# Kernel tuning notes

Hardware: AMD Instinct MI355X
Metric: run time of the kernel (lower is better)

## Reference

```python
import jax, jax.numpy as jnp
import numpy as np

B, N, C = 16, 1025, 1024
H, D = 16, 64          # num_heads, head_dim
NPT = 1                # num_prefix_tokens
EPS = 1e-6
SCALE = D ** -0.5


def layer_norm(x, g, b, eps=EPS):
    mu = jnp.mean(x, axis=-1, keepdims=True)
    var = jnp.mean(jnp.square(x - mu), axis=-1, keepdims=True)
    return (x - mu) * jax.lax.rsqrt(var + eps) * g + b


def rot(x):
    # interleaved rotate-half: out[..., ::2] = -x[..., 1::2]; out[..., 1::2] = x[..., ::2]
    x2 = x.reshape(*x.shape[:-1], -1, 2)
    return jnp.stack([-x2[..., 1], x2[..., 0]], axis=-1).reshape(x.shape)


def apply_rot_embed_cat(x, emb):
    # emb: (N_spatial, 2*D) = [sin | cos]
    sin_emb, cos_emb = jnp.split(emb, 2, axis=-1)
    return x * cos_emb + rot(x) * sin_emb


def setup_inputs() -> dict:
    key = jax.random.key(0)
    ks = jax.random.split(key, 12)
    s = 0.02
    return {
        "x": jax.random.normal(ks[0], (B, N, C), jnp.float32),
        "rope": jax.random.normal(ks[1], (N - NPT, 2 * D), jnp.float32),
        "qkv_w": jax.random.normal(ks[2], (3 * C, C), jnp.float32) * s,
        "q_bias": jax.random.normal(ks[3], (C,), jnp.float32) * s,
        "k_bias": jnp.zeros((C,), jnp.float32),  # registered buffer, always zero
        "v_bias": jax.random.normal(ks[4], (C,), jnp.float32) * s,
        "qn_g": jnp.ones((D,), jnp.float32),
        "qn_b": jnp.zeros((D,), jnp.float32),
        "kn_g": jnp.ones((D,), jnp.float32),
        "kn_b": jnp.zeros((D,), jnp.float32),
        "norm_g": jnp.ones((C,), jnp.float32),
        "norm_b": jnp.zeros((C,), jnp.float32),
        "proj_w": jax.random.normal(ks[5], (C, C), jnp.float32) * s,
        "proj_b": jnp.zeros((C,), jnp.float32),
    }


def reference(x, rope, qkv_w, q_bias, k_bias, v_bias, qn_g, qn_b, kn_g, kn_b,
              norm_g, norm_b, proj_w, proj_b):
    b, n, c = x.shape
    qkv_bias = jnp.concatenate([q_bias, k_bias, v_bias])
    qkv = jnp.einsum('bnc,oc->bno', x, qkv_w) + qkv_bias          # (B,N,3C)
    qkv = qkv.reshape(b, n, 3, H, D).transpose(2, 0, 3, 1, 4)     # (3,B,H,N,D)
    q, k, v = qkv[0], qkv[1], qkv[2]
    # per-head QK layernorm over head_dim
    q = layer_norm(q, qn_g, qn_b)
    k = layer_norm(k, kn_g, kn_b)
    # RoPE on spatial tokens only (prefix tokens excluded)
    q = jnp.concatenate([q[:, :, :NPT], apply_rot_embed_cat(q[:, :, NPT:], rope)], axis=2)
    k = jnp.concatenate([k[:, :, :NPT], apply_rot_embed_cat(k[:, :, NPT:], rope)], axis=2)
    # scaled dot product attention
    attn = jnp.einsum('bhqd,bhkd->bhqk', q * SCALE, k)
    attn = jax.nn.softmax(attn, axis=-1)
    out = jnp.einsum('bhqk,bhkd->bhqd', attn, v)                  # (B,H,N,D)
    out = out.transpose(0, 2, 1, 3).reshape(b, n, c)              # (B,N,C)
    out = layer_norm(out, norm_g, norm_b)                         # scale_norm
    out = jnp.einsum('bnc,oc->bno', out, proj_w) + proj_b
    return out
```

## Files before the change

kernel.cpp:

```cpp
#include <hip/hip_runtime.h>
#include <hip/hip_bf16.h>

#define B_ 16
#define N_ 1025
#define C_ 1024
#define H_ 16
#define D_ 64
#define M_ (B_ * N_)
#define EPS_ 1e-6f
#define SCALE_ 0.125f
#define VTS_ 1088

typedef __attribute__((ext_vector_type(8))) short bf16x8;
typedef __attribute__((ext_vector_type(4))) float f32x4;
typedef unsigned short u16;
typedef unsigned int u32;

__device__ inline float bf2f(u16 h) {
    union { u32 u; float f; } c; c.u = ((u32)h) << 16; return c.f;
}
__device__ inline u16 f2bf(float f) {
    union { u32 u; float f; } c; c.f = f;
    u32 r = c.u + 0x7FFF + ((c.u >> 16) & 1);
    return (u16)(r >> 16);
}
__device__ inline u32 cvtpk(float lo, float hi) {
    u32 r;
    asm("v_cvt_pk_bf16_f32 %0, %1, %2" : "=v"(r) : "v"(lo), "v"(hi));
    return r;
}

__device__ inline void gload16(const void* g, void* l) {
    __builtin_amdgcn_global_load_lds(
        (const __attribute__((address_space(1))) void*)g,
        (__attribute__((address_space(3))) void*)l, 16, 0, 0);
}

__global__ void k_sniff(const u32* __restrict__ norm_g_bits, int* __restrict__ flag)
{
    if (threadIdx.x == 0 && blockIdx.x == 0)
        flag[0] = (norm_g_bits[0] == 0x3F800000u) ? 1 : 0;
}

__global__ __launch_bounds__(256) void k_convert(
    const void* __restrict__ src, u16* __restrict__ dst, long n,
    const int* __restrict__ flag)
{
    const int f = flag[0];
    long i0 = ((long)blockIdx.x * 256 + threadIdx.x) * 4;
    long stride = (long)gridDim.x * 1024;
    if (f) {
        const float* s = (const float*)src;
        for (long i = i0; i < n; i += stride) {
#pragma unroll
            for (int j = 0; j < 4; ++j) dst[i + j] = f2bf(s[i + j]);
        }
    } else {
        const u16* s = (const u16*)src;
        for (long i = i0; i < n; i += stride) {
#pragma unroll
            for (int j = 0; j < 4; ++j) dst[i + j] = s[i + j];
        }
    }
}

__global__ __launch_bounds__(256) void k_convert_small(
    const void* s0, const void* s1, const void* s2, const void* s3,
    const void* s4, const void* s5, const void* s6, const void* s7,
    const void* s8, const void* s9, u16* __restrict__ dst,
    const int* __restrict__ flag)
{
    int i = blockIdx.x * 256 + threadIdx.x;
    if (i >= 6400) return;
    const void* src; int off;
    if      (i < 1024) { src = s0; off = i; }
    else if (i < 2048) { src = s1; off = i - 1024; }
    else if (i < 3072) { src = s2; off = i - 2048; }
    else if (i < 3136) { src = s3; off = i - 3072; }
    else if (i < 3200) { src = s4; off = i - 3136; }
    else if (i < 3264) { src = s5; off = i - 3200; }
    else if (i < 3328) { src = s6; off = i - 3264; }
    else if (i < 4352) { src = s7; off = i - 3328; }
    else if (i < 5376) { src = s8; off = i - 4352; }
    else               { src = s9; off = i - 5376; }
    dst[i] = flag[0] ? f2bf(((const float*)src)[off]) : ((const u16*)src)[off];
}

__global__ __launch_bounds__(256) void k_qkv(
    const u16* __restrict__ x, const u16* __restrict__ wmat,
    const u16* __restrict__ qbias, const u16* __restrict__ kbias,
    const u16* __restrict__ vbias,
    u16* __restrict__ q, u16* __restrict__ kk, u16* __restrict__ vv)
{
    __shared__ __attribute__((aligned(16))) u16 As[128 * 32];
    __shared__ __attribute__((aligned(16))) u16 Bs[128 * 32];
    const int t  = threadIdx.x;
    const int m0 = blockIdx.y * 128;
    const int n0 = blockIdx.x * 128;
    const int w  = t >> 6;
    const int ln = t & 15;
    const int qd = (t & 63) >> 4;
    const int wr = (w >> 1) * 64;
    const int wc = (w & 1) * 64;

    f32x4 acc[4][4] = {};

    const int srow = t >> 2;
    const int scol = (t & 3) * 8;
    int ar0 = m0 + srow;       if (ar0 >= M_) ar0 = M_ - 1;
    int ar1 = m0 + 64 + srow;  if (ar1 >= M_) ar1 = M_ - 1;
    const u16* ap0 = x + (size_t)ar0 * C_ + scol;
    const u16* ap1 = x + (size_t)ar1 * C_ + scol;
    const u16* bp0 = wmat + (size_t)(n0 + srow) * C_ + scol;
    const u16* bp1 = wmat + (size_t)(n0 + 64 + srow) * C_ + scol;
    u16* lA0 = &As[t * 8];
    u16* lA1 = &As[2048 + t * 8];
    u16* lB0 = &Bs[t * 8];
    u16* lB1 = &Bs[2048 + t * 8];

    for (int k0 = 0; k0 < C_; k0 += 32) {
        gload16(ap0 + k0, lA0);
        gload16(ap1 + k0, lA1);
        gload16(bp0 + k0, lB0);
        gload16(bp1 + k0, lB1);
        __syncthreads();
        bf16x8 a[4], b[4];
#pragma unroll
        for (int i = 0; i < 4; ++i)
            a[i] = *(const bf16x8*)&As[(wr + i * 16 + ln) * 32 + qd * 8];
#pragma unroll
        for (int j = 0; j < 4; ++j)
            b[j] = *(const bf16x8*)&Bs[(wc + j * 16 + ln) * 32 + qd * 8];
#pragma unroll
        for (int i = 0; i < 4; ++i)
#pragma unroll
            for (int j = 0; j < 4; ++j)
                acc[i][j] = __builtin_amdgcn_mfma_f32_16x16x32_bf16(a[i], b[j], acc[i][j], 0, 0, 0);
        __syncthreads();
    }

#pragma unroll
    for (int j = 0; j < 4; ++j) {
        int o = n0 + wc + j * 16 + ln;
        int part = o >> 10;
        int c = o & 1023;
        int h = c >> 6, d = c & 63;
        const u16* bias = (part == 0) ? qbias : (part == 1) ? kbias : vbias;
        u16* dst = (part == 0) ? q : (part == 1) ? kk : vv;
        float bv = bf2f(bias[c]);
#pragma unroll
        for (int i = 0; i < 4; ++i) {
#pragma unroll
            for (int r = 0; r < 4; ++r) {
                int m = m0 + wr + i * 16 + qd * 4 + r;
                if (m >= M_) continue;
                int bb = m / N_, n = m % N_;
                dst[(((size_t)(bb * H_ + h)) * N_ + n) * D_ + d] = f2bf(acc[i][j][r] + bv);
            }
        }
    }
}

__global__ __launch_bounds__(256) void k_lnrope(
    u16* __restrict__ buf, const u16* __restrict__ g, const u16* __restrict__ bt,
    const u16* __restrict__ rope, float scale)
{
    int wid = (blockIdx.x * 256 + threadIdx.x) >> 6;
    int d = threadIdx.x & 63;
    if (wid >= B_ * H_ * N_) return;
    int n = wid % N_;
    u16* row = buf + (size_t)wid * 64;

    float xv = bf2f(row[d]);
    float s = xv;
#pragma unroll
    for (int off = 32; off; off >>= 1) s += __shfl_xor(s, off);
    float mu = s * (1.f / 64.f);
    float dv = xv - mu;
    float s2 = dv * dv;
#pragma unroll
    for (int off = 32; off; off >>= 1) s2 += __shfl_xor(s2, off);
    float var = s2 * (1.f / 64.f);
    float y = dv * rsqrtf(var + EPS_) * bf2f(g[d]) + bf2f(bt[d]);

    if (n >= 1) {
        const u16* rp = rope + (size_t)(n - 1) * 128;
        float sn = bf2f(rp[d]);
        float cs = bf2f(rp[64 + d]);
        float part = __shfl_xor(y, 1);
        float rot = (d & 1) ? part : -part;
        y = y * cs + rot * sn;
    }
    row[d] = f2bf(y * scale);
}

__global__ __launch_bounds__(256) void k_vt(
    const u16* __restrict__ v, u16* __restrict__ vt)
{
    const int kb = blockIdx.x % 17;
    const int bh = blockIdx.x / 17;
    const int k0 = kb * 64;
    const size_t src = (size_t)bh * N_ * D_;
    const size_t dst = (size_t)bh * D_ * VTS_;
    const int t = threadIdx.x;
    const int d = t & 63;
    const int kg0 = t >> 6;
#pragma unroll
    for (int c = 0; c < 2; ++c) {
        int kg = kg0 + c * 4;
        bf16x8 pk;
#pragma unroll
        for (int i = 0; i < 8; ++i) {
            int gk = k0 + kg * 8 + i; if (gk > N_ - 1) gk = N_ - 1;
            pk[i] = (short)v[src + (size_t)gk * D_ + d];
        }
        *(bf16x8*)(vt + dst + (size_t)d * VTS_ + k0 + kg * 8) = pk;
    }
}

__global__ __launch_bounds__(256) void k_attn(
    const u16* __restrict__ q, const u16* __restrict__ k,
    const u16* __restrict__ vt, u16* __restrict__ out)
{
    __shared__ __attribute__((aligned(16))) u16 Ks[64 * 72];
    __shared__ __attribute__((aligned(16))) u16 Vs[64 * 72];
    __shared__ __attribute__((aligned(16))) u16 Pt[4][2][16 * 72];

    const int t  = threadIdx.x;
    const int w  = t >> 6;
    const int ln = t & 15;
    const int qd = (t & 63) >> 4;

    const int qb = blockIdx.x % 9;
    const int bh = blockIdx.x / 9;
    const int b = bh >> 4, h = bh & 15;
    const size_t kbase = (size_t)bh * N_ * D_;
    const size_t vbase = (size_t)bh * D_ * VTS_;
    const int qw = qb * 128 + w * 32;

    bf16x8 qa[2][2];
#pragma unroll
    for (int a = 0; a < 2; ++a) {
        int row = qw + a * 16 + ln; if (row > N_ - 1) row = N_ - 1;
        const u16* qp = q + kbase + (size_t)row * D_;
        qa[a][0] = *(const bf16x8*)(qp + qd * 8);
        qa[a][1] = *(const bf16x8*)(qp + 32 + qd * 8);
    }

    f32x4 o_acc[2][4] = {};
    float m_run[2] = { -1e30f, -1e30f };
    float l_run[2] = { 0.f, 0.f };

    const int skey = t >> 3;
    const int sdg  = t & 7;

    bf16x8 pk[2], pv[2];
#pragma unroll
    for (int c = 0; c < 2; ++c) {
        int r32 = c * 32 + skey;
        pk[c] = *(const bf16x8*)(k + kbase + (size_t)r32 * D_ + sdg * 8);
        pv[c] = *(const bf16x8*)(vt + vbase + (size_t)r32 * VTS_ + sdg * 8);
    }

    for (int k0 = 0; k0 < N_; k0 += 64) {
#pragma unroll
        for (int c = 0; c < 2; ++c) {
            int r32 = c * 32 + skey;
            *(bf16x8*)&Ks[r32 * 72 + sdg * 8] = pk[c];
            *(bf16x8*)&Vs[r32 * 72 + sdg * 8] = pv[c];
        }
        __syncthreads();

        const int k1 = k0 + 64;
        if (k1 < N_) {
#pragma unroll
            for (int c = 0; c < 2; ++c) {
                int r32 = c * 32 + skey;
                int gk = k1 + r32; if (gk > N_ - 1) gk = N_ - 1;
                pk[c] = *(const bf16x8*)(k + kbase + (size_t)gk * D_ + sdg * 8);
                pv[c] = *(const bf16x8*)(vt + vbase + (size_t)r32 * VTS_ + k1 + sdg * 8);
            }
        }

        bf16x8 kf[4][2];
#pragma unroll
        for (int ks = 0; ks < 4; ++ks) {
            kf[ks][0] = *(const bf16x8*)&Ks[(ks * 16 + ln) * 72 + qd * 8];
            kf[ks][1] = *(const bf16x8*)&Ks[(ks * 16 + ln) * 72 + 32 + qd * 8];
        }

        f32x4 s2[2][4] = {};
        __builtin_amdgcn_s_setprio(1);
#pragma unroll
        for (int a = 0; a < 2; ++a)
#pragma unroll
            for (int ks = 0; ks < 4; ++ks) {
                s2[a][ks] = __builtin_amdgcn_mfma_f32_16x16x32_bf16(kf[ks][0], qa[a][0], s2[a][ks], 0, 0, 0);
                s2[a][ks] = __builtin_amdgcn_mfma_f32_16x16x32_bf16(kf[ks][1], qa[a][1], s2[a][ks], 0, 0, 0);
            }
        __builtin_amdgcn_s_setprio(0);

        if (k0 + 64 > N_) {
#pragma unroll
            for (int a = 0; a < 2; ++a)
#pragma unroll
                for (int ks = 0; ks < 4; ++ks)
#pragma unroll
                    for (int r = 0; r < 4; ++r)
                        if (k0 + 16 * ks + 4 * qd + r > N_ - 1) s2[a][ks][r] = -1e30f;
        }

        float mx[2];
#pragma unroll
        for (int a = 0; a < 2; ++a) {
            float t0 = fmaxf(fmaxf(s2[a][0][0], s2[a][0][1]), fmaxf(s2[a][0][2], s2[a][0][3]));
            float t1 = fmaxf(fmaxf(s2[a][1][0], s2[a][1][1]), fmaxf(s2[a][1][2], s2[a][1][3]));
            float t2 = fmaxf(fmaxf(s2[a][2][0], s2[a][2][1]), fmaxf(s2[a][2][2], s2[a][2][3]));
            float t3 = fmaxf(fmaxf(s2[a][3][0], s2[a][3][1]), fmaxf(s2[a][3][2], s2[a][3][3]));
            float m = fmaxf(fmaxf(t0, t1), fmaxf(t2, t3));
            m = fmaxf(m, __shfl_xor(m, 16));
            m = fmaxf(m, __shfl_xor(m, 32));
            mx[a] = m;
        }

#pragma unroll
        for (int a = 0; a < 2; ++a) {
            if (__any(mx[a] > m_run[a])) {
                float mn = fmaxf(m_run[a], mx[a]);
                float al = __expf(m_run[a] - mn);
                m_run[a] = mn;
                l_run[a] *= al;
#pragma unroll
                for (int nt = 0; nt < 4; ++nt)
#pragma unroll
                    for (int r = 0; r < 4; ++r)
                        o_acc[a][nt][r] *= al;
            }
            const float mcur = m_run[a];
            float rs = 0.f;
#pragma unroll
            for (int ks = 0; ks < 4; ++ks)
#pragma unroll
                for (int r = 0; r < 4; ++r) {
                    s2[a][ks][r] = __expf(s2[a][ks][r] - mcur);
                    rs += s2[a][ks][r];
                }
            rs += __shfl_xor(rs, 16);
            rs += __shfl_xor(rs, 32);
            l_run[a] += rs;

            u16* pt = &Pt[w][a][0];
#pragma unroll
            for (int ks = 0; ks < 4; ++ks) {
                *(u32*)&pt[ln * 72 + 16 * ks + 4 * qd]     = cvtpk(s2[a][ks][0], s2[a][ks][1]);
                *(u32*)&pt[ln * 72 + 16 * ks + 4 * qd + 2] = cvtpk(s2[a][ks][2], s2[a][ks][3]);
            }
        }

        bf16x8 pf[2][2];
#pragma unroll
        for (int a = 0; a < 2; ++a) {
            const u16* pt = &Pt[w][a][0];
            pf[a][0] = *(const bf16x8*)&pt[ln * 72 + qd * 8];
            pf[a][1] = *(const bf16x8*)&pt[ln * 72 + 32 + qd * 8];
        }

        __builtin_amdgcn_s_setprio(1);
#pragma unroll
        for (int nt = 0; nt < 4; ++nt) {
            bf16x8 v0 = *(const bf16x8*)&Vs[(nt * 16 + ln) * 72 + qd * 8];
            bf16x8 v1 = *(const bf16x8*)&Vs[(nt * 16 + ln) * 72 + 32 + qd * 8];
#pragma unroll
            for (int a = 0; a < 2; ++a) {
                o_acc[a][nt] = __builtin_amdgcn_mfma_f32_16x16x32_bf16(v0, pf[a][0], o_acc[a][nt], 0, 0, 0);
                o_acc[a][nt] = __builtin_amdgcn_mfma_f32_16x16x32_bf16(v1, pf[a][1], o_acc[a][nt], 0, 0, 0);
            }
        }
        __builtin_amdgcn_s_setprio(0);
        __syncthreads();
    }

#pragma unroll
    for (int a = 0; a < 2; ++a) {
        int n = qw + a * 16 + ln;
        if (n >= N_) continue;
        float lr = l_run[a];
        u16* op = out + ((size_t)b * N_ + n) * C_ + h * 64;
#pragma unroll
        for (int nt = 0; nt < 4; ++nt)
#pragma unroll
            for (int rp = 0; rp < 2; ++rp) {
                int d = nt * 16 + qd * 4 + rp * 2;
                *(u32*)&op[d] = cvtpk(o_acc[a][nt][rp * 2] / lr,
                                      o_acc[a][nt][rp * 2 + 1] / lr);
            }
    }
}

__global__ __launch_bounds__(256) void k_ln(
    const u16* __restrict__ in, const u16* __restrict__ g,
    const u16* __restrict__ bt, u16* __restrict__ outb)
{
    __shared__ float red[8];
    const int row = blockIdx.x;
    const int t = threadIdx.x;
    const u16* p = in + (size_t)row * C_;

    float vals[4];
    float s = 0.f;
#pragma unroll
    for (int i = 0; i < 4; ++i) { vals[i] = bf2f(p[t + i * 256]); s += vals[i]; }
#pragma unroll
    for (int off = 32; off; off >>= 1) s += __shfl_xor(s, off);
    if ((t & 63) == 0) red[t >> 6] = s;
    __syncthreads();
    float mu = (red[0] + red[1] + red[2] + red[3]) * (1.f / 1024.f);
    float s2 = 0.f;
#pragma unroll
    for (int i = 0; i < 4; ++i) { float d = vals[i] - mu; s2 += d * d; }
#pragma unroll
    for (int off = 32; off; off >>= 1) s2 += __shfl_xor(s2, off);
    __syncthreads();
    if ((t & 63) == 0) red[t >> 6] = s2;
    __syncthreads();
    float var = (red[0] + red[1] + red[2] + red[3]) * (1.f / 1024.f);
    float rs = rsqrtf(var + EPS_);
#pragma unroll
    for (int i = 0; i < 4; ++i) {
        int cidx = t + i * 256;
        float y = (vals[i] - mu) * rs * bf2f(g[cidx]) + bf2f(bt[cidx]);
        outb[(size_t)row * C_ + cidx] = f2bf(y);
    }
}

__global__ __launch_bounds__(256) void k_proj(
    const u16* __restrict__ y, const u16* __restrict__ wmat,
    const u16* __restrict__ bias, void* __restrict__ out,
    const int* __restrict__ flag)
{
    __shared__ __attribute__((aligned(16))) u16 As[128 * 32];
    __shared__ __attribute__((aligned(16))) u16 Bs[128 * 32];
    const int t  = threadIdx.x;
    const int m0 = blockIdx.y * 128;
    const int n0 = blockIdx.x * 128;
    const int w  = t >> 6;
    const int ln = t & 15;
    const int qd = (t & 63) >> 4;
    const int wr = (w >> 1) * 64;
    const int wc = (w & 1) * 64;

    f32x4 acc[4][4] = {};

    const int srow = t >> 2;
    const int scol = (t & 3) * 8;
    int ar0 = m0 + srow;       if (ar0 >= M_) ar0 = M_ - 1;
    int ar1 = m0 + 64 + srow;  if (ar1 >= M_) ar1 = M_ - 1;
    const u16* ap0 = y + (size_t)ar0 * C_ + scol;
    const u16* ap1 = y + (size_t)ar1 * C_ + scol;
    const u16* bp0 = wmat + (size_t)(n0 + srow) * C_ + scol;
    const u16* bp1 = wmat + (size_t)(n0 + 64 + srow) * C_ + scol;
    u16* lA0 = &As[t * 8];
    u16* lA1 = &As[2048 + t * 8];
    u16* lB0 = &Bs[t * 8];
    u16* lB1 = &Bs[2048 + t * 8];

    for (int k0 = 0; k0 < C_; k0 += 32) {
        gload16(ap0 + k0, lA0);
        gload16(ap1 + k0, lA1);
        gload16(bp0 + k0, lB0);
        gload16(bp1 + k0, lB1);
        __syncthreads();
        bf16x8 a[4], b[4];
#pragma unroll
        for (int i = 0; i < 4; ++i)
            a[i] = *(const bf16x8*)&As[(wr + i * 16 + ln) * 32 + qd * 8];
#pragma unroll
        for (int j = 0; j < 4; ++j)
            b[j] = *(const bf16x8*)&Bs[(wc + j * 16 + ln) * 32 + qd * 8];
#pragma unroll
        for (int i = 0; i < 4; ++i)
#pragma unroll
            for (int j = 0; j < 4; ++j)
                acc[i][j] = __builtin_amdgcn_mfma_f32_16x16x32_bf16(a[i], b[j], acc[i][j], 0, 0, 0);
        __syncthreads();
    }

    const int f32out = flag[0];
#pragma unroll
    for (int j = 0; j < 4; ++j) {
        int o = n0 + wc + j * 16 + ln;
        float bv = bf2f(bias[o]);
#pragma unroll
        for (int i = 0; i < 4; ++i) {
#pragma unroll
            for (int r = 0; r < 4; ++r) {
                int m = m0 + wr + i * 16 + qd * 4 + r;
                if (m >= M_) continue;
                float val = acc[i][j][r] + bv;
                if (f32out) ((float*)out)[(size_t)m * C_ + o] = val;
                else        ((u16*)out)[(size_t)m * C_ + o] = f2bf(val);
            }
        }
    }
}

extern "C" void kernel_launch(void* const* d_in, const int* in_sizes, int n_in,
                              void* d_out, int out_size, void* d_ws, size_t ws_size,
                              hipStream_t stream)
{
    char* ws = (char*)d_ws;
    int* flag = (int*)ws;
    u16* arena = (u16*)(ws + 256);

    const long X_OFF = 0,            X_N = (long)M_ * C_;
    const long R_OFF = X_OFF + X_N,  R_N = (long)(N_ - 1) * 2 * D_;
    const long W_OFF = R_OFF + R_N,  W_N = (long)3 * C_ * C_;
    const long P_OFF = W_OFF + W_N,  P_N = (long)C_ * C_;
    const long S_OFF = P_OFF + P_N;
    const long ARENA_N = S_OFF + 6400;

    u16* xb   = arena + X_OFF;
    u16* ropb = arena + R_OFF;
    u16* qkvw = arena + W_OFF;
    u16* pw   = arena + P_OFF;
    u16* qb   = arena + S_OFF;
    u16* kb   = qb + 1024;
    u16* vb   = kb + 1024;
    u16* qng  = vb + 1024;
    u16* qnb  = qng + 64;
    u16* kng  = qnb + 64;
    u16* knb  = kng + 64;
    u16* ng   = knb + 64;
    u16* nb   = ng + 1024;
    u16* pb   = nb + 1024;

    char* after = (char*)(arena + ARENA_N);
    const size_t sz = (size_t)B_ * H_ * N_ * D_ * 2;
    u16* qbuf = (u16*)after;
    u16* kbuf = (u16*)(after + sz);
    u16* vbuf = (u16*)(after + 2 * sz);
    u16* vtb  = (u16*)(after + 3 * sz);
    u16* ao   = xb;
    u16* ybuf = qbuf;

    k_sniff<<<1, 64, 0, stream>>>((const u32*)d_in[10], flag);

    k_convert<<<4096, 256, 0, stream>>>(d_in[0], xb, X_N, flag);
    k_convert<<<128, 256, 0, stream>>>(d_in[1], ropb, R_N, flag);
    k_convert<<<2048, 256, 0, stream>>>(d_in[2], qkvw, W_N, flag);
    k_convert<<<1024, 256, 0, stream>>>(d_in[12], pw, P_N, flag);
    k_convert_small<<<25, 256, 0, stream>>>(
        d_in[3], d_in[4], d_in[5], d_in[6], d_in[7], d_in[8], d_in[9],
        d_in[10], d_in[11], d_in[13], qb, flag);

    dim3 g1(24, 129);
    k_qkv<<<g1, 256, 0, stream>>>(xb, qkvw, qb, kb, vb, qbuf, kbuf, vbuf);

    const int rows = B_ * H_ * N_;
    k_lnrope<<<(rows + 3) / 4, 256, 0, stream>>>(qbuf, qng, qnb, ropb, SCALE_);
    k_lnrope<<<(rows + 3) / 4, 256, 0, stream>>>(kbuf, kng, knb, ropb, 1.0f);

    k_vt<<<B_ * H_ * 17, 256, 0, stream>>>(vbuf, vtb);

    k_attn<<<B_ * H_ * 9, 256, 0, stream>>>(qbuf, kbuf, vtb, ao);

    k_ln<<<M_, 256, 0, stream>>>(ao, ng, nb, ybuf);

    dim3 g2(8, 129);
    k_proj<<<g2, 256, 0, stream>>>(ybuf, pw, pb, d_out, flag);
}
```

Before: 665.7 us.

## Transpose V through swizzled LDS, regroup attention blocks, zero-init MFMA accumulators

The V transpose kernel now loads coalesced 16-byte rows into a swizzled shared-memory tile and writes transposed vectors from there, replacing the strided per-element global reads. The attention kernel remaps block indices so that consecutive blocks cover eight different heads at the same query block, which changes L2 locality for K/V. The first QK MFMA of each tile now takes a zero constant as its accumulator instead of a zero-initialised register array, saving the register zeroing. The transpose gains a barrier and LDS traffic, and the block remap may help or hurt cache reuse.

```diff
diff --git a/kernel.cpp b/kernel.cpp
--- a/kernel.cpp
+++ b/kernel.cpp
@@ -197,24 +197,39 @@
 __global__ __launch_bounds__(256) void k_vt(
     const u16* __restrict__ v, u16* __restrict__ vt)
 {
+    __shared__ __attribute__((aligned(16))) u16 T[64 * 72];
     const int kb = blockIdx.x % 17;
     const int bh = blockIdx.x / 17;
     const int k0 = kb * 64;
     const size_t src = (size_t)bh * N_ * D_;
     const size_t dst = (size_t)bh * D_ * VTS_;
     const int t = threadIdx.x;
-    const int d = t & 63;
-    const int kg0 = t >> 6;
+
 #pragma unroll
     for (int c = 0; c < 2; ++c) {
-        int kg = kg0 + c * 4;
+        int id = c * 256 + t;
+        int gk = id >> 3;
+        int d0 = (id & 7) * 8;
+        int gka = k0 + gk; if (gka > N_ - 1) gka = N_ - 1;
+        bf16x8 x = *(const bf16x8*)(v + src + (size_t)gka * D_ + d0);
+        int col = d0 ^ (8 * ((gk & 7) ^ (gk >> 3)));
+        *(bf16x8*)&T[gk * 72 + col] = x;
+    }
+    __syncthreads();
+
+#pragma unroll
+    for (int c = 0; c < 2; ++c) {
+        int id = c * 256 + t;
+        int d   = id >> 3;
+        int kk0 = (id & 7) * 8;
         bf16x8 pk;
 #pragma unroll
-        for (int i = 0; i < 8; ++i) {
-            int gk = k0 + kg * 8 + i; if (gk > N_ - 1) gk = N_ - 1;
-            pk[i] = (short)v[src + (size_t)gk * D_ + d];
-        }
-        *(bf16x8*)(vt + dst + (size_t)d * VTS_ + k0 + kg * 8) = pk;
+        for (int j = 0; j < 8; ++j) {
+            int key = kk0 + j;
+            int col = d ^ (8 * ((key & 7) ^ (key >> 3)));
+            pk[j] = (short)T[key * 72 + col];
+        }
+        *(bf16x8*)(vt + dst + (size_t)d * VTS_ + k0 + kk0) = pk;
     }
 }
 
@@ -231,11 +246,12 @@
     const int ln = t & 15;
     const int qd = (t & 63) >> 4;
 
-    const int qb = blockIdx.x % 9;
-    const int bh = blockIdx.x / 9;
-    const int b = bh >> 4, h = bh & 15;
-    const size_t kbase = (size_t)bh * N_ * D_;
-    const size_t vbase = (size_t)bh * D_ * VTS_;
+    const int p  = blockIdx.x;
+    const int g  = (p & 7) + 8 * ((p >> 3) / 9);
+    const int qb = (p >> 3) % 9;
+    const int b = g >> 4, h = g & 15;
+    const size_t kbase = (size_t)g * N_ * D_;
+    const size_t vbase = (size_t)g * D_ * VTS_;
     const int qw = qb * 128 + w * 32;
 
     bf16x8 qa[2][2];
@@ -250,6 +266,7 @@
     f32x4 o_acc[2][4] = {};
     float m_run[2] = { -1e30f, -1e30f };
     float l_run[2] = { 0.f, 0.f };
+    const f32x4 zf = { 0.f, 0.f, 0.f, 0.f };
 
     const int skey = t >> 3;
     const int sdg  = t & 7;
@@ -289,13 +306,13 @@
             kf[ks][1] = *(const bf16x8*)&Ks[(ks * 16 + ln) * 72 + 32 + qd * 8];
         }
 
-        f32x4 s2[2][4] = {};
+        f32x4 s2[2][4];
         __builtin_amdgcn_s_setprio(1);
 #pragma unroll
         for (int a = 0; a < 2; ++a)
 #pragma unroll
             for (int ks = 0; ks < 4; ++ks) {
-                s2[a][ks] = __builtin_amdgcn_mfma_f32_16x16x32_bf16(kf[ks][0], qa[a][0], s2[a][ks], 0, 0, 0);
+                s2[a][ks] = __builtin_amdgcn_mfma_f32_16x16x32_bf16(kf[ks][0], qa[a][0], zf, 0, 0, 0);
                 s2[a][ks] = __builtin_amdgcn_mfma_f32_16x16x32_bf16(kf[ks][1], qa[a][1], s2[a][ks], 0, 0, 0);
             }
         __builtin_amdgcn_s_setprio(0);
```

Result: no change. 670.8 us (+0.8%).
